# Performance work log

Measured on AMD Instinct MI355X. Metric: run time of the kernel, lower is better.

Reference implementation:

```python
import jax, jax.numpy as jnp
import numpy as np

jax.config.update("jax_enable_x64", True)


def expand_bits_10(v):
    # v: uint32 with values in [0, 1023]; spread bits 2 apart (30-bit result)
    x = v.astype(jnp.uint32)
    x = (x | (x << 16)) & jnp.uint32(0x030000FF)
    x = (x | (x << 8)) & jnp.uint32(0x0300F00F)
    x = (x | (x << 4)) & jnp.uint32(0x030C30C3)
    x = (x | (x << 2)) & jnp.uint32(0x09249249)
    return x


def encode_morton(x, y, z):
    xc = jnp.clip(x, 0, 1023).astype(jnp.uint32)
    yc = jnp.clip(y, 0, 1023).astype(jnp.uint32)
    zc = jnp.clip(z, 0, 1023).astype(jnp.uint32)
    return (expand_bits_10(xc) << 2) | (expand_bits_10(yc) << 1) | expand_bits_10(zc)


def setup_inputs() -> dict:
    key = jax.random.key(0)
    k1, k2 = jax.random.split(key)
    M = 500_000
    WORLD = 512.0
    centers = jax.random.uniform(k1, (M, 3), jnp.float32, 0.0, WORLD)
    radii = jax.random.uniform(k2, (M, 1), jnp.float32, 0.2, 1.5)
    return {
        "min_corners": centers - radii,
        "max_corners": centers + radii,
        "global_min": jnp.zeros((3,), jnp.float32),
        "voxel_size": jnp.ones((1,), jnp.float32),
        "grid_size": 512,
        "oversized_threshold": 64,
    }


def reference(min_corners, max_corners, global_min, voxel_size, grid_size, oversized_threshold):
    M = min_corners.shape[0]
    T = oversized_threshold  # max voxels per non-oversized sphere (pad width)
    vs = voxel_size.reshape(())

    def gcoord(p):  # world -> clipped grid coordinate, [M,3] int32
        g = jnp.floor((p - global_min[None, :]) / vs).astype(jnp.int32)
        return jnp.clip(g, 0, grid_size - 1)

    g_min = gcoord(min_corners)
    g_max = gcoord(max_corners)
    extent = g_max - g_min + 1  # [M,3]
    num_vox = extent[:, 0] * extent[:, 1] * extent[:, 2]

    # Pass 1: per-sphere voxel counts, oversized flags
    is_oversized = (num_vox > oversized_threshold).astype(jnp.int32)
    counts = jnp.where(is_oversized == 1, 0, num_vox).astype(jnp.int32)
    offsets = jnp.concatenate(
        [jnp.zeros((1,), jnp.int32), jnp.cumsum(counts).astype(jnp.int32)]
    )  # [M+1] CSR offsets
    total_pairs = offsets[-1]

    # Pass 2: enumerate padded sphere-voxel pairs. Linear index k decomposes
    # into (dx, dy, dz) exactly like the kernel's triple loop (z fastest).
    k = jnp.arange(T, dtype=jnp.int32)[None, :]          # [1,T]
    ez = extent[:, 2:3]
    ey = extent[:, 1:2]
    dz = k % ez
    dy = (k // ez) % ey
    dx = k // (ez * ey)
    valid = k < counts[:, None]                            # [M,T]

    gx = g_min[:, 0:1] + dx
    gy = g_min[:, 1:2] + dy
    gz = g_min[:, 2:3] + dz
    morton = encode_morton(gx, gy, gz).astype(jnp.int64)   # [M,T]

    SENTINEL = jnp.int64(1) << 40  # > any 30-bit morton; sorts to the end
    morton = jnp.where(valid, morton, SENTINEL)
    sid = jnp.where(valid, jnp.arange(M, dtype=jnp.int32)[:, None], -1)

    flat_m = morton.reshape(-1)
    flat_s = sid.reshape(-1)
    order = jnp.argsort(flat_m)  # stable; valid pairs form the sorted prefix
    pairs_morton = flat_m[order]
    pairs_sphere_id = flat_s[order]

    return pairs_morton, pairs_sphere_id, offsets, is_oversized, total_pairs
```

## Files before the change

kernel.cpp:

```cpp
#include <hip/hip_runtime.h>
#include <stdint.h>

typedef uint16_t u16;
typedef uint32_t u32;
typedef uint64_t u64;

#define TPB   256
#define TILE  2048
#define RADIX 512
#define RBITS 9
#define STILE 4096
#define GSPB  256

#define SCTPB 512
#define NWAVE 8
#define SSLOT 8
#define NXCD  8

__device__ __forceinline__ int clampi(int v, int lo, int hi){ return v < lo ? lo : (v > hi ? hi : v); }

__device__ __forceinline__ u32 expand10(u32 x){
  x &= 1023u;
  x = (x | (x << 16)) & 0x030000FFu;
  x = (x | (x << 8))  & 0x0300F00Fu;
  x = (x | (x << 4))  & 0x030C30C3u;
  x = (x | (x << 2))  & 0x09249249u;
  return x;
}

struct Box { int a0,a1,a2,e0,e1,e2,nv; };
__device__ __forceinline__ Box boxOf(int i, const float* mn, const float* mx,
                                     float g0, float g1, float g2, float vs, int gs){
  Box b;
  int a0 = clampi((int)floorf((mn[3*i+0] - g0) / vs), 0, gs-1);
  int a1 = clampi((int)floorf((mn[3*i+1] - g1) / vs), 0, gs-1);
  int a2 = clampi((int)floorf((mn[3*i+2] - g2) / vs), 0, gs-1);
  int b0 = clampi((int)floorf((mx[3*i+0] - g0) / vs), 0, gs-1);
  int b1 = clampi((int)floorf((mx[3*i+1] - g1) / vs), 0, gs-1);
  int b2 = clampi((int)floorf((mx[3*i+2] - g2) / vs), 0, gs-1);
  b.a0=a0; b.a1=a1; b.a2=a2;
  b.e0=b0-a0+1; b.e1=b1-a1+1; b.e2=b2-a2+1;
  b.nv = b.e0*b.e1*b.e2;
  return b;
}

__global__ void countK(const float* mn, const float* mx, const float* gmin,
                       const float* vs_p, const int* gs_p, const int* T_p,
                       u32* counts, int* out_ovr, uint4* boxEnc, int M){
  int i = blockIdx.x * TPB + threadIdx.x;
  if (i >= M) return;
  float vs = vs_p[0]; int gs = gs_p[0]; int T = T_p[0];
  Box b = boxOf(i, mn, mx, gmin[0], gmin[1], gmin[2], vs, gs);
  int ovr = b.nv > T;
  counts[i] = ovr ? 0u : (u32)b.nv;
  out_ovr[i] = ovr;
  u32 nvq = ovr ? 0u : (u32)b.nv;
  uint4 be;
  be.x = (u32)b.a0 | ((u32)b.a1 << 10) | ((u32)b.a2 << 20);
  be.y = (u32)b.e1 | ((u32)b.e2 << 7) | (nvq << 14);
  be.z = 65535u / (u32)b.e1 + 1u;
  be.w = 65535u / (u32)b.e2 + 1u;
  boxEnc[i] = be;
}

__global__ void scanAK(const u32* counts, int* out_off, u32* blockSums, int M){
  __shared__ u32 s[TPB];
  int b = blockIdx.x, t = threadIdx.x;
  int base = b * TILE + t * 8;
  u32 incl[8]; u32 run = 0;
  #pragma unroll
  for (int j = 0; j < 8; ++j){
    int g = base + j;
    u32 v = (g < M) ? counts[g] : 0u;
    run += v; incl[j] = run;
  }
  s[t] = run;
  __syncthreads();
  for (int o = 1; o < TPB; o <<= 1){
    u32 x = (t >= o) ? s[t-o] : 0u;
    __syncthreads();
    s[t] += x;
    __syncthreads();
  }
  u32 tbase = s[t] - run;
  #pragma unroll
  for (int j = 0; j < 8; ++j){
    int g = base + j;
    if (g < M) out_off[g+1] = (int)(tbase + incl[j]);
  }
  if (t == TPB-1) blockSums[b] = s[TPB-1];
}

__global__ void scanBK(u32* blockSums, int nb){
  __shared__ u32 s[TPB];
  int t = threadIdx.x;
  u32 run = 0;
  int nch = (nb + TPB - 1) / TPB;
  for (int c = 0; c < nch; ++c){
    int i = c * TPB + t;
    u32 v = (i < nb) ? blockSums[i] : 0u;
    s[t] = v;
    __syncthreads();
    for (int o = 1; o < TPB; o <<= 1){
      u32 x = (t >= o) ? s[t-o] : 0u;
      __syncthreads();
      s[t] += x;
      __syncthreads();
    }
    if (i < nb) blockSums[i] = run + s[t] - v;
    u32 tot = s[TPB-1];
    __syncthreads();
    run += tot;
  }
}

__global__ void scanCK(int* out_off, const u32* blockSums, int M, int* out_total){
  int b = blockIdx.x, t = threadIdx.x;
  u32 add = blockSums[b];
  int base = b * TILE + t * 8;
  #pragma unroll
  for (int j = 0; j < 8; ++j){
    int g = base + j;
    if (g < M){
      int v = out_off[g+1] + (int)add;
      out_off[g+1] = v;
      if (g == M-1) out_total[0] = v;
    }
  }
  if (b == 0 && t == 0) out_off[0] = 0;
}

__global__ void genK(const uint4* __restrict__ boxEnc, const int* __restrict__ out_off,
                     u64* __restrict__ out, int M){
  int t = threadIdx.x;
  int lane = t & 63, wave = t >> 6;
  int half = lane >> 5, l32 = lane & 31;
  int sbase = blockIdx.x * GSPB;
  int slot = wave * 2 + half;
  for (int s0 = 0; s0 < GSPB; s0 += 8){
    int i = sbase + s0 + slot;
    if (i >= M) continue;
    uint4 be = boxEnc[i];
    int nv = (int)(be.y >> 14);
    if (nv == 0) continue;
    int ey = (int)(be.y & 127), ez = (int)((be.y >> 7) & 127);
    int a0 = (int)(be.x & 1023), a1 = (int)((be.x >> 10) & 1023), a2 = (int)(be.x >> 20);
    u32 mEy = be.z, mEz = be.w;
    int base = out_off[i];
    for (int k = l32; k < nv; k += 32){
      u32 q1 = ((u32)k * mEz) >> 16;
      int dz = k - (int)(q1 * (u32)ez);
      u32 q2 = (q1 * mEy) >> 16;
      int dy = (int)q1 - (int)(q2 * (u32)ey);
      int dx = (int)q2;
      u32 m = (expand10((u32)(a0 + dx)) << 2) |
              (expand10((u32)(a1 + dy)) << 1) |
               expand10((u32)(a2 + dz));
      out[base + k] = ((u64)m << 32) | (u32)i;
    }
  }
}

__global__ void histK(const u64* __restrict__ in, u32* hist,
                      const int* total_p, int maxTiles, int shift){
  __shared__ u32 cnt[RADIX];
  int tile = blockIdx.x, t = threadIdx.x;
  int total = *total_p;
  int numTiles = (total + STILE - 1) / STILE;
  if (tile >= numTiles) return;
  cnt[t] = 0; cnt[t + TPB] = 0;
  __syncthreads();
  int base = tile * STILE;
  if (base + STILE <= total){
    const uint4* k4 = (const uint4*)(in + base);
    #pragma unroll
    for (int s = 0; s < 8; ++s){
      uint4 v = k4[s * TPB + t];
      atomicAdd(&cnt[(v.y >> shift) & (RADIX-1)], 1u);
      atomicAdd(&cnt[(v.w >> shift) & (RADIX-1)], 1u);
    }
  } else {
    const u32* hi = (const u32*)in;
    #pragma unroll
    for (int s = 0; s < 16; ++s){
      int j = base + s * TPB + t;
      if (j < total) atomicAdd(&cnt[(hi[2*j+1] >> shift) & (RADIX-1)], 1u);
    }
  }
  __syncthreads();
  for (int d = t; d < RADIX; d += TPB)
    hist[(size_t)d * maxTiles + tile] = cnt[d];
}

__global__ void tileScanK(u32* hist, u32* digitTotal, const int* total_p, int maxTiles){
  __shared__ u32 s[TPB];
  int d = blockIdx.x, t = threadIdx.x;
  int total = *total_p;
  int numTiles = (total + STILE - 1) / STILE;
  u32 running = 0;
  int nch = (numTiles + TPB - 1) / TPB;
  for (int c = 0; c < nch; ++c){
    int i = c * TPB + t;
    u32 v = (i < numTiles) ? hist[(size_t)d * maxTiles + i] : 0u;
    s[t] = v;
    __syncthreads();
    for (int o = 1; o < TPB; o <<= 1){
      u32 x = (t >= o) ? s[t-o] : 0u;
      __syncthreads();
      s[t] += x;
      __syncthreads();
    }
    if (i < numTiles) hist[(size_t)d * maxTiles + i] = running + s[t] - v;
    u32 tot = s[TPB-1];
    __syncthreads();
    running += tot;
  }
  if (t == 0) digitTotal[d] = running;
}

__global__ void digitScanK(const u32* digitTotal, u32* digitBase){
  __shared__ u32 s[RADIX];
  int t = threadIdx.x;
  u32 v = digitTotal[t];
  s[t] = v;
  __syncthreads();
  for (int o = 1; o < RADIX; o <<= 1){
    u32 x = (t >= o) ? s[t-o] : 0u;
    __syncthreads();
    s[t] += x;
    __syncthreads();
  }
  digitBase[t] = s[t] - v;
}

__global__ __launch_bounds__(SCTPB, 4)
void scatterK(const u64* __restrict__ in, u64* __restrict__ out,
              const u32* __restrict__ hist, const u32* __restrict__ digitBase,
              const int* total_p, int maxTiles, int shift){
  __shared__ u64 stage[STILE];
  __shared__ u16 wHist[NWAVE * RADIX];
  __shared__ u32 startS[RADIX];
  __shared__ u32 baseS[RADIX];

  int t = threadIdx.x;
  int total = *total_p;
  int numTiles = (total + STILE - 1) / STILE;

  int bid = blockIdx.x;
  int q = numTiles / NXCD, r = numTiles % NXCD;
  int x = bid & (NXCD - 1), pos = bid >> 3;
  int cnt_x = q + (x < r ? 1 : 0);
  if (pos >= cnt_x) return;
  int tile = (x < r ? x * (q + 1) : r * (q + 1) + (x - r) * q) + pos;

  int lane = t & 63, wave = t >> 6;
  u64 lt = (1ull << lane) - 1ull;
  u16* wh = &wHist[wave << 9];

  for (int i = t; i < NWAVE * RADIX; i += SCTPB) wHist[i] = 0;
  __syncthreads();

  int tbase = tile * STILE;
  int cbase = tbase + (wave << 9);
  u64 relem[SSLOT];
  u32 rrd[SSLOT];

  #pragma unroll
  for (int s = 0; s < SSLOT; ++s){
    int idx = cbase + (s << 6) + lane;
    bool valid = idx < total;
    u64 e = valid ? in[idx] : 0ull;
    relem[s] = e;
    int d = (int)(((u32)(e >> 32)) >> shift) & (RADIX - 1);
    u64 mask = __ballot(valid);
    #pragma unroll
    for (int b = 0; b < RBITS; ++b){
      u64 bal = __ballot((d >> b) & 1);
      mask &= ((d >> b) & 1) ? bal : ~bal;
    }
    u32 lr = (u32)__popcll(mask & lt);
    u32 old = valid ? (u32)wh[d] : 0u;
    if (valid && ((mask & lt) == 0ull)) wh[d] = (u16)(old + (u32)__popcll(mask));
    rrd[s] = ((old + lr) << 16) | (u32)d;
  }
  __syncthreads();

  {
    int d = t;
    u32 run = 0;
    #pragma unroll
    for (int wv = 0; wv < NWAVE; ++wv){
      u32 cc = wHist[(wv << 9) + d];
      wHist[(wv << 9) + d] = (u16)run;
      run += cc;
    }
    startS[d] = run;
  }
  __syncthreads();

  {
    u32 v = startS[t];
    baseS[t] = v;
    __syncthreads();
    for (int o = 1; o < RADIX; o <<= 1){
      u32 xv = (t >= o) ? baseS[t-o] : 0u;
      __syncthreads();
      baseS[t] += xv;
      __syncthreads();
    }
    u32 excl = baseS[t] - v;
    __syncthreads();
    startS[t] = excl;
    baseS[t] = digitBase[t] + hist[(size_t)t * maxTiles + tile];
  }
  __syncthreads();

  #pragma unroll
  for (int s = 0; s < SSLOT; ++s){
    int idx = cbase + (s << 6) + lane;
    if (idx < total){
      u32 rd = rrd[s];
      u32 d = rd & (RADIX - 1);
      u32 p = startS[d] + (u32)wh[d] + (rd >> 16);
      stage[p] = relem[s];
    }
  }
  __syncthreads();

  int tileElems = total - tbase; if (tileElems > STILE) tileElems = STILE;
  for (int j = t; j < tileElems; j += SCTPB){
    u64 e = stage[j];
    u32 key = (u32)(e >> 32);
    int d = (int)((key >> shift) & (RADIX - 1));
    int dest = (int)(baseS[d] + (u32)j - startS[d]);
    out[dest] = e;
  }
}

__global__ void unzipTailK(const u64* __restrict__ buf, int* out_m, int* out_s,
                           const int* total_p, int MT){
  int total = *total_p;
  int base = blockIdx.x * 8192 + threadIdx.x * 4;
  #pragma unroll
  for (int s = 0; s < 8; ++s){
    int j = base + s * 1024;
    if (j + 3 < MT && (j + 3 < total || j >= total)){
      uint4 vm, vsid;
      if (j + 3 < total){
        u64 e0 = buf[j], e1 = buf[j+1], e2 = buf[j+2], e3 = buf[j+3];
        vm   = make_uint4((u32)(e0 >> 32), (u32)(e1 >> 32), (u32)(e2 >> 32), (u32)(e3 >> 32));
        vsid = make_uint4((u32)e0, (u32)e1, (u32)e2, (u32)e3);
      } else {
        vm   = make_uint4(0u, 0u, 0u, 0u);
        vsid = make_uint4(0xFFFFFFFFu, 0xFFFFFFFFu, 0xFFFFFFFFu, 0xFFFFFFFFu);
      }
      *(uint4*)&out_m[j] = vm;
      *(uint4*)&out_s[j] = vsid;
    } else if (j < MT){
      int end = (j + 4 < MT) ? j + 4 : MT;
      for (int k = j; k < end; ++k){
        if (k < total){
          u64 e = buf[k];
          out_m[k] = (int)(u32)(e >> 32);
          out_s[k] = (int)(u32)e;
        } else {
          out_m[k] = 0;
          out_s[k] = -1;
        }
      }
    }
  }
}

extern "C" void kernel_launch(void* const* d_in, const int* in_sizes, int n_in,
                              void* d_out, int out_size, void* d_ws, size_t ws_size,
                              hipStream_t stream){
  const float* mn   = (const float*)d_in[0];
  const float* mx   = (const float*)d_in[1];
  const float* gmin = (const float*)d_in[2];
  const float* vs   = (const float*)d_in[3];
  const int*   gs   = (const int*)d_in[4];
  const int*   T_p  = (const int*)d_in[5];

  int M = in_sizes[0] / 3;
  long long S = (long long)out_size - 2LL*M - 2LL;
  int T = (int)(S / (2LL*M));
  int MT = (int)((long long)M * T);

  int* out_m     = (int*)d_out;
  int* out_s     = out_m + MT;
  int* out_off   = out_s + MT;
  int* out_ovr   = out_off + (M + 1);
  int* out_total = out_ovr + M;

  uint8_t* w = (uint8_t*)d_ws;
  size_t off = 0;
  auto alloc = [&](size_t bytes) -> void* {
    size_t p = (off + 255) & ~(size_t)255;
    off = p + bytes;
    return (void*)(w + p);
  };
  int nbA = (M + TILE - 1) / TILE;
  u32*   counts     = (u32*)alloc((size_t)M * 4);
  uint4* boxEnc     = (uint4*)alloc((size_t)M * 16);
  u32*   blockSums  = (u32*)alloc((size_t)nbA * 4);
  u32*   digitTotal = (u32*)alloc(RADIX * 4);
  u32*   digitBase  = (u32*)alloc(RADIX * 4);

  size_t fixed = off + 8192;
  size_t avail = ws_size > fixed ? ws_size - fixed : 0;
  long long cap = (long long)(avail / 14) & ~(long long)(STILE - 1);
  if (cap > MT) cap = MT;
  if (cap < STILE) cap = STILE;
  int maxTiles = (int)(cap / STILE);

  size_t histSz = (size_t)RADIX * maxTiles * 4;
  u32* hist0 = (u32*)alloc(histSz);
  u32* hist1 = (u32*)alloc(histSz);
  u32* hist2 = (u32*)alloc(histSz);
  u64* bufA  = (u64*)alloc((size_t)cap * 8);

  u64* bufB = (u64*)d_out;

  int gM = (M + TPB - 1) / TPB;
  int gGen = (M + GSPB - 1) / GSPB;

  countK<<<gM, TPB, 0, stream>>>(mn, mx, gmin, vs, gs, T_p, counts, out_ovr, boxEnc, M);
  scanAK<<<nbA, TPB, 0, stream>>>(counts, out_off, blockSums, M);
  scanBK<<<1, TPB, 0, stream>>>(blockSums, nbA);
  scanCK<<<nbA, TPB, 0, stream>>>(out_off, blockSums, M, out_total);
  genK<<<gGen, TPB, 0, stream>>>(boxEnc, out_off, bufB, M);

  histK<<<maxTiles, TPB, 0, stream>>>(bufB, hist0, out_total, maxTiles, 0);
  tileScanK<<<RADIX, TPB, 0, stream>>>(hist0, digitTotal, out_total, maxTiles);
  digitScanK<<<1, RADIX, 0, stream>>>(digitTotal, digitBase);
  scatterK<<<maxTiles, SCTPB, 0, stream>>>(bufB, bufA, hist0, digitBase, out_total, maxTiles, 0);

  histK<<<maxTiles, TPB, 0, stream>>>(bufA, hist1, out_total, maxTiles, RBITS);
  tileScanK<<<RADIX, TPB, 0, stream>>>(hist1, digitTotal, out_total, maxTiles);
  digitScanK<<<1, RADIX, 0, stream>>>(digitTotal, digitBase);
  scatterK<<<maxTiles, SCTPB, 0, stream>>>(bufA, bufB, hist1, digitBase, out_total, maxTiles, RBITS);

  histK<<<maxTiles, TPB, 0, stream>>>(bufB, hist2, out_total, maxTiles, 2*RBITS);
  tileScanK<<<RADIX, TPB, 0, stream>>>(hist2, digitTotal, out_total, maxTiles);
  digitScanK<<<1, RADIX, 0, stream>>>(digitTotal, digitBase);
  scatterK<<<maxTiles, SCTPB, 0, stream>>>(bufB, bufA, hist2, digitBase, out_total, maxTiles, 2*RBITS);

  unzipTailK<<<(MT + 8191) / 8192, TPB, 0, stream>>>(bufA, out_m, out_s, out_total, MT);
}
```

Measured before the change: 419.0 us.

## Fuse first-pass radix histogram into generation and fold digit scan into scatter

The pair generation kernel now builds the digit-0 per-tile histogram itself. It counts into a shared-memory window of tiles and flushes to global memory with atomics, which removes the first histogram kernel and its full read of the generated keys. The separate single-block digit-prefix kernel is also removed: each scatter block now does a combined 64-bit scan that packs the global digit totals with its local tile counts. This trades three kernel launches and one pass over memory for atomics in the generator, redundant digit scans in every scatter block, and an extra memset of the histogram.

```diff
diff --git a/kernel.cpp b/kernel.cpp
--- a/kernel.cpp
+++ b/kernel.cpp
@@ -11,6 +11,7 @@
 #define RBITS 9
 #define STILE 4096
 #define GSPB  256
+#define WIN   6
 
 #define SCTPB 512
 #define NWAVE 8
@@ -131,11 +132,17 @@
 }
 
 __global__ void genK(const uint4* __restrict__ boxEnc, const int* __restrict__ out_off,
-                     u64* __restrict__ out, int M){
+                     u64* __restrict__ out, u32* hist0, int maxTiles, int M){
+  __shared__ u32 winHist[WIN * RADIX];
+  __shared__ int stile0;
   int t = threadIdx.x;
+  for (int i = t; i < WIN * RADIX; i += TPB) winHist[i] = 0;
+  int sbase = blockIdx.x * GSPB;
+  if (t == 0) stile0 = out_off[sbase] >> 12;
+  __syncthreads();
+  int tile0 = stile0;
   int lane = t & 63, wave = t >> 6;
   int half = lane >> 5, l32 = lane & 31;
-  int sbase = blockIdx.x * GSPB;
   int slot = wave * 2 + half;
   for (int s0 = 0; s0 < GSPB; s0 += 8){
     int i = sbase + s0 + slot;
@@ -156,7 +163,20 @@
       u32 m = (expand10((u32)(a0 + dx)) << 2) |
               (expand10((u32)(a1 + dy)) << 1) |
                expand10((u32)(a2 + dz));
-      out[base + k] = ((u64)m << 32) | (u32)i;
+      int pos = base + k;
+      out[pos] = ((u64)m << 32) | (u32)i;
+      u32 d0 = m & (RADIX - 1);
+      int rel = (pos >> 12) - tile0;
+      if ((unsigned)rel < WIN) atomicAdd(&winHist[(rel << 9) + d0], 1u);
+      else atomicAdd(&hist0[(size_t)d0 * maxTiles + (pos >> 12)], 1u);
+    }
+  }
+  __syncthreads();
+  for (int idx = t; idx < WIN * RADIX; idx += TPB){
+    u32 c = winHist[idx];
+    if (c){
+      int wnd = idx >> 9, d = idx & (RADIX - 1);
+      atomicAdd(&hist0[(size_t)d * maxTiles + (tile0 + wnd)], c);
     }
   }
 }
@@ -218,24 +238,9 @@
   if (t == 0) digitTotal[d] = running;
 }
 
-__global__ void digitScanK(const u32* digitTotal, u32* digitBase){
-  __shared__ u32 s[RADIX];
-  int t = threadIdx.x;
-  u32 v = digitTotal[t];
-  s[t] = v;
-  __syncthreads();
-  for (int o = 1; o < RADIX; o <<= 1){
-    u32 x = (t >= o) ? s[t-o] : 0u;
-    __syncthreads();
-    s[t] += x;
-    __syncthreads();
-  }
-  digitBase[t] = s[t] - v;
-}
-
 __global__ __launch_bounds__(SCTPB, 4)
 void scatterK(const u64* __restrict__ in, u64* __restrict__ out,
-              const u32* __restrict__ hist, const u32* __restrict__ digitBase,
+              const u32* __restrict__ hist, const u32* __restrict__ digitTotal,
               const int* total_p, int maxTiles, int shift){
   __shared__ u64 stage[STILE];
   __shared__ u16 wHist[NWAVE * RADIX];
@@ -285,6 +290,7 @@
   }
   __syncthreads();
 
+  u32 tileCnt;
   {
     int d = t;
     u32 run = 0;
@@ -294,24 +300,24 @@
       wHist[(wv << 9) + d] = (u16)run;
       run += cc;
     }
-    startS[d] = run;
+    tileCnt = run;
   }
   __syncthreads();
 
   {
-    u32 v = startS[t];
-    baseS[t] = v;
+    u64 v = ((u64)digitTotal[t] << 32) | (u64)tileCnt;
+    stage[t] = v;
     __syncthreads();
     for (int o = 1; o < RADIX; o <<= 1){
-      u32 xv = (t >= o) ? baseS[t-o] : 0u;
-      __syncthreads();
-      baseS[t] += xv;
-      __syncthreads();
-    }
-    u32 excl = baseS[t] - v;
-    __syncthreads();
-    startS[t] = excl;
-    baseS[t] = digitBase[t] + hist[(size_t)t * maxTiles + tile];
+      u64 xv = (t >= o) ? stage[t-o] : 0ull;
+      __syncthreads();
+      stage[t] += xv;
+      __syncthreads();
+    }
+    u64 excl = stage[t] - v;
+    __syncthreads();
+    startS[t] = (u32)excl;
+    baseS[t]  = (u32)(excl >> 32) + hist[(size_t)t * maxTiles + tile];
   }
   __syncthreads();
 
@@ -405,7 +411,6 @@
   uint4* boxEnc     = (uint4*)alloc((size_t)M * 16);
   u32*   blockSums  = (u32*)alloc((size_t)nbA * 4);
   u32*   digitTotal = (u32*)alloc(RADIX * 4);
-  u32*   digitBase  = (u32*)alloc(RADIX * 4);
 
   size_t fixed = off + 8192;
   size_t avail = ws_size > fixed ? ws_size - fixed : 0;
@@ -425,26 +430,23 @@
   int gM = (M + TPB - 1) / TPB;
   int gGen = (M + GSPB - 1) / GSPB;
 
+  hipMemsetAsync(hist0, 0, histSz, stream);
   countK<<<gM, TPB, 0, stream>>>(mn, mx, gmin, vs, gs, T_p, counts, out_ovr, boxEnc, M);
   scanAK<<<nbA, TPB, 0, stream>>>(counts, out_off, blockSums, M);
   scanBK<<<1, TPB, 0, stream>>>(blockSums, nbA);
   scanCK<<<nbA, TPB, 0, stream>>>(out_off, blockSums, M, out_total);
-  genK<<<gGen, TPB, 0, stream>>>(boxEnc, out_off, bufB, M);
-
-  histK<<<maxTiles, TPB, 0, stream>>>(bufB, hist0, out_total, maxTiles, 0);
+  genK<<<gGen, TPB, 0, stream>>>(boxEnc, out_off, bufB, hist0, maxTiles, M);
+
   tileScanK<<<RADIX, TPB, 0, stream>>>(hist0, digitTotal, out_total, maxTiles);
-  digitScanK<<<1, RADIX, 0, stream>>>(digitTotal, digitBase);
-  scatterK<<<maxTiles, SCTPB, 0, stream>>>(bufB, bufA, hist0, digitBase, out_total, maxTiles, 0);
+  scatterK<<<maxTiles, SCTPB, 0, stream>>>(bufB, bufA, hist0, digitTotal, out_total, maxTiles, 0);
 
   histK<<<maxTiles, TPB, 0, stream>>>(bufA, hist1, out_total, maxTiles, RBITS);
   tileScanK<<<RADIX, TPB, 0, stream>>>(hist1, digitTotal, out_total, maxTiles);
-  digitScanK<<<1, RADIX, 0, stream>>>(digitTotal, digitBase);
-  scatterK<<<maxTiles, SCTPB, 0, stream>>>(bufA, bufB, hist1, digitBase, out_total, maxTiles, RBITS);
+  scatterK<<<maxTiles, SCTPB, 0, stream>>>(bufA, bufB, hist1, digitTotal, out_total, maxTiles, RBITS);
 
   histK<<<maxTiles, TPB, 0, stream>>>(bufB, hist2, out_total, maxTiles, 2*RBITS);
   tileScanK<<<RADIX, TPB, 0, stream>>>(hist2, digitTotal, out_total, maxTiles);
-  digitScanK<<<1, RADIX, 0, stream>>>(digitTotal, digitBase);
-  scatterK<<<maxTiles, SCTPB, 0, stream>>>(bufB, bufA, hist2, digitBase, out_total, maxTiles, 2*RBITS);
+  scatterK<<<maxTiles, SCTPB, 0, stream>>>(bufB, bufA, hist2, digitTotal, out_total, maxTiles, 2*RBITS);
 
   unzipTailK<<<(MT + 8191) / 8192, TPB, 0, stream>>>(bufA, out_m, out_s, out_total, MT);
 }
```

Result: slower. 470.4 us (+12.3%).
